# Kernel tuning notes

Hardware: AMD Instinct MI355X
Metric: run time of the kernel (lower is better)

The kernel has to match this reference:

```python
import jax, jax.numpy as jnp
import numpy as np

B, D, H, W = 16, 256, 32, 32
M = 2048


def setup_inputs() -> dict:
    key = jax.random.key(0)
    kz, ke = jax.random.split(key)
    z = jax.random.normal(kz, (B, D, H, W), dtype=jnp.float32)
    e = jax.random.normal(ke, (M, D), dtype=jnp.float32)
    return {"z": z, "e": e}


def reference(z, e):
    # flatten (B, D, H, W) -> (N, D), matching permute(0,2,3,1).reshape(-1, D)
    zf = jnp.transpose(z, (0, 2, 3, 1)).reshape(-1, z.shape[1])  # (N, D)
    # squared L2 distance via GEMM expansion: ||z||^2 + ||e||^2 - 2 z.e^T
    z_sq = jnp.sum(zf * zf, axis=1, keepdims=True)        # (N, 1)
    e_sq = jnp.sum(e * e, axis=1)                          # (M,)
    cross = jnp.einsum('nd,md->nm', zf, e)                 # (N, M)
    distance = jnp.maximum(z_sq + e_sq[None, :] - 2.0 * cross, 0.0)  # (N, M)
    # loss: mean over codes of min over flattened z vectors (min along dim 0)
    loss = jnp.mean(jnp.min(distance, axis=0))
    return distance, loss
```

## Files before the change

### kernel.cpp

```cpp
#include <hip/hip_runtime.h>

typedef __attribute__((ext_vector_type(8))) short bf16x8;
typedef __attribute__((ext_vector_type(4))) float f32x4;

#define NTOT 16384
#define MCODES 2048
#define DDIM 256

__device__ __forceinline__ unsigned short f2bf(float f) {
  union { float f; unsigned u; } v; v.f = f;
  unsigned r = v.u + 0x7FFFu + ((v.u >> 16) & 1u);
  return (unsigned short)(r >> 16);
}
__device__ __forceinline__ float bf2f(unsigned short u) {
  union { unsigned u; float f; } v; v.u = ((unsigned)u) << 16;
  return v.f;
}

#define GLOAD16(gptr, lptr) \
  __builtin_amdgcn_global_load_lds((const __attribute__((address_space(1))) void*)(gptr), \
                                   (__attribute__((address_space(3))) void*)(lptr), 16, 0, 0)

__global__ void prep_e_k(const float* __restrict__ e, unsigned short* __restrict__ ebf,
                         float* __restrict__ esq, unsigned* __restrict__ colmin) {
  int row = blockIdx.x * 4 + (threadIdx.x >> 6);
  int lane = threadIdx.x & 63;
  const float4 v = *(const float4*)(e + (size_t)row * DDIM + lane * 4);
  ushort4 o;
  o.x = f2bf(v.x); o.y = f2bf(v.y); o.z = f2bf(v.z); o.w = f2bf(v.w);
  *(ushort4*)(ebf + (size_t)row * DDIM + lane * 4) = o;
  float s = v.x * v.x + v.y * v.y + v.z * v.z + v.w * v.w;
  #pragma unroll
  for (int off = 32; off; off >>= 1) s += __shfl_xor(s, off, 64);
  if (lane == 0) {
    esq[row] = s;
    colmin[row] = 0x7F800000u;
  }
}

__global__ void transpose_z_k(const float* __restrict__ z, unsigned short* __restrict__ zf) {
  __shared__ float t[64][68];
  const int b = blockIdx.z, d0 = blockIdx.x * 64, hw0 = blockIdx.y * 64;
  const int l16 = threadIdx.x & 15, g = threadIdx.x >> 4;
  const float* src = z + (size_t)b * 262144 + (size_t)d0 * 1024 + hw0;
  #pragma unroll
  for (int it = 0; it < 4; ++it) {
    int dl = it * 16 + g;
    float4 v = *(const float4*)(src + (size_t)dl * 1024 + l16 * 4);
    *(float4*)&t[dl][l16 * 4] = v;
  }
  __syncthreads();
  const int dl4 = (threadIdx.x & 15) * 4, hwl = threadIdx.x >> 4;
  unsigned short* dst = zf + ((size_t)b * 1024 + hw0) * DDIM + d0;
  #pragma unroll
  for (int it = 0; it < 4; ++it) {
    int hw = it * 16 + hwl;
    float a0 = t[dl4 + 0][hw], a1 = t[dl4 + 1][hw];
    float a2 = t[dl4 + 2][hw], a3 = t[dl4 + 3][hw];
    uint2 w;
    w.x = (unsigned)f2bf(a0) | ((unsigned)f2bf(a1) << 16);
    w.y = (unsigned)f2bf(a2) | ((unsigned)f2bf(a3) << 16);
    *(uint2*)(dst + (size_t)hw * DDIM + dl4) = w;
  }
}

__global__ void zsq_k(const unsigned short* __restrict__ zf, float* __restrict__ zsq) {
  int row = blockIdx.x * 4 + (threadIdx.x >> 6);
  int lane = threadIdx.x & 63;
  ushort4 v = *(const ushort4*)(zf + (size_t)row * DDIM + lane * 4);
  float a = bf2f(v.x), b = bf2f(v.y), c = bf2f(v.z), d = bf2f(v.w);
  float s = a * a + b * b + c * c + d * d;
  #pragma unroll
  for (int off = 32; off; off >>= 1) s += __shfl_xor(s, off, 64);
  if (lane == 0) zsq[row] = s;
}

__global__ __launch_bounds__(256) void gemm_k(
    const unsigned short* __restrict__ A,
    const unsigned short* __restrict__ B,
    const float* __restrict__ zsq, const float* __restrict__ esq,
    unsigned* __restrict__ colmin, float* __restrict__ out) {
  __shared__ unsigned short As[128 * 32];
  __shared__ unsigned short Bs[128 * 32];
  const int wave = threadIdx.x >> 6, lane = threadIdx.x & 63;
  const int wm = wave >> 1, wn = wave & 1;
  const int row0 = blockIdx.y * 128, col0 = blockIdx.x * 128;

  f32x4 acc[4][4] = {};

  const int sr = wave * 16 + (lane >> 2);
  const int sc = (lane & 3) * 8;
  const size_t aBase = (size_t)(row0 + sr) * DDIM + sc;
  const size_t bBase = (size_t)(col0 + sr) * DDIM + sc;

  for (int k0 = 0; k0 < DDIM; k0 += 32) {
    GLOAD16(A + aBase + k0, As + wave * 512);
    GLOAD16(A + aBase + k0 + (size_t)64 * DDIM, As + wave * 512 + 64 * 32);
    GLOAD16(B + bBase + k0, Bs + wave * 512);
    GLOAD16(B + bBase + k0 + (size_t)64 * DDIM, Bs + wave * 512 + 64 * 32);
    __syncthreads();

    bf16x8 a[4], b[4];
    #pragma unroll
    for (int i = 0; i < 4; ++i)
      a[i] = *(const bf16x8*)(As + (wm * 64 + i * 16 + (lane & 15)) * 32 + (lane >> 4) * 8);
    #pragma unroll
    for (int j = 0; j < 4; ++j)
      b[j] = *(const bf16x8*)(Bs + (wn * 64 + j * 16 + (lane & 15)) * 32 + (lane >> 4) * 8);
    #pragma unroll
    for (int i = 0; i < 4; ++i)
      #pragma unroll
      for (int j = 0; j < 4; ++j)
        acc[i][j] = __builtin_amdgcn_mfma_f32_16x16x32_bf16(a[i], b[j], acc[i][j], 0, 0, 0);
    __syncthreads();
  }

  const int r0 = lane >> 4, c = lane & 15;
  float cmin[4] = {3.4e38f, 3.4e38f, 3.4e38f, 3.4e38f};
  #pragma unroll
  for (int j = 0; j < 4; ++j) {
    const int col = col0 + wn * 64 + j * 16 + c;
    const float es = esq[col];
    #pragma unroll
    for (int i = 0; i < 4; ++i) {
      const int row = row0 + wm * 64 + i * 16 + r0 * 4;
      const float4 zs = *(const float4*)(zsq + row);
      const float d0 = fmaxf(zs.x + es - 2.0f * acc[i][j][0], 0.0f);
      const float d1 = fmaxf(zs.y + es - 2.0f * acc[i][j][1], 0.0f);
      const float d2 = fmaxf(zs.z + es - 2.0f * acc[i][j][2], 0.0f);
      const float d3 = fmaxf(zs.w + es - 2.0f * acc[i][j][3], 0.0f);
      out[(size_t)(row + 0) * MCODES + col] = d0;
      out[(size_t)(row + 1) * MCODES + col] = d1;
      out[(size_t)(row + 2) * MCODES + col] = d2;
      out[(size_t)(row + 3) * MCODES + col] = d3;
      cmin[j] = fminf(cmin[j], fminf(fminf(d0, d1), fminf(d2, d3)));
    }
  }
  #pragma unroll
  for (int j = 0; j < 4; ++j) {
    float m = cmin[j];
    m = fminf(m, __shfl_xor(m, 16, 64));
    m = fminf(m, __shfl_xor(m, 32, 64));
    if (lane < 16) {
      const int col = col0 + wn * 64 + j * 16 + lane;
      atomicMin(colmin + col, __float_as_uint(m));
    }
  }
}

__global__ void loss_k(const unsigned* __restrict__ colmin, float* __restrict__ loss) {
  __shared__ float sdata[4];
  int t = threadIdx.x;
  float s = 0.0f;
  for (int i = t; i < MCODES; i += 256) s += __uint_as_float(colmin[i]);
  #pragma unroll
  for (int off = 32; off; off >>= 1) s += __shfl_down(s, off, 64);
  if ((t & 63) == 0) sdata[t >> 6] = s;
  __syncthreads();
  if (t == 0) loss[0] = (sdata[0] + sdata[1] + sdata[2] + sdata[3]) * (1.0f / (float)MCODES);
}

extern "C" void kernel_launch(void* const* d_in, const int* in_sizes, int n_in,
                              void* d_out, int out_size, void* d_ws, size_t ws_size,
                              hipStream_t stream) {
  const float* z = (const float*)d_in[0];
  const float* e = (const float*)d_in[1];
  float* out = (float*)d_out;

  float* ws = (float*)d_ws;
  float* zsq = ws;
  float* esq = ws + NTOT;
  unsigned* colmin = (unsigned*)(ws + NTOT + MCODES);
  unsigned short* ebf = (unsigned short*)(ws + NTOT + 2 * MCODES);
  unsigned short* zf = ebf + (size_t)MCODES * DDIM;

  prep_e_k<<<MCODES / 4, 256, 0, stream>>>(e, ebf, esq, colmin);
  transpose_z_k<<<dim3(4, 16, 16), 256, 0, stream>>>(z, zf);
  zsq_k<<<NTOT / 4, 256, 0, stream>>>(zf, zsq);
  gemm_k<<<dim3(MCODES / 128, NTOT / 128), 256, 0, stream>>>(zf, ebf, zsq, esq, colmin, out);
  loss_k<<<1, 256, 0, stream>>>(colmin, out + (size_t)NTOT * MCODES);
}
```

Before: 181.7 us.

## Fuse z-norm into transpose, double-buffer GEMM LDS with swizzle, nontemporal stores

Folds the z squared-norm computation into the transpose kernel, which now accumulates per-row sums with atomicAdd into a zsq buffer zeroed in prep_e_k. This removes a separate kernel launch and a re-read of zf. It also changes the squared norm to use the fp32 values instead of the rounded bf16 ones. The GEMM now uses a double-buffered LDS pipeline with a K tile of 64 and an XOR swizzle against bank conflicts, plus launch bounds for two blocks per CU. Output distances are written with nontemporal stores to avoid polluting the cache with the large output.

Result: no change. 184.6 us (+1.6%).

```diff
diff --git a/kernel.cpp b/kernel.cpp
--- a/kernel.cpp
+++ b/kernel.cpp
@@ -12,17 +12,15 @@
   unsigned r = v.u + 0x7FFFu + ((v.u >> 16) & 1u);
   return (unsigned short)(r >> 16);
 }
-__device__ __forceinline__ float bf2f(unsigned short u) {
-  union { unsigned u; float f; } v; v.u = ((unsigned)u) << 16;
-  return v.f;
-}
 
 #define GLOAD16(gptr, lptr) \
   __builtin_amdgcn_global_load_lds((const __attribute__((address_space(1))) void*)(gptr), \
                                    (__attribute__((address_space(3))) void*)(lptr), 16, 0, 0)
 
 __global__ void prep_e_k(const float* __restrict__ e, unsigned short* __restrict__ ebf,
-                         float* __restrict__ esq, unsigned* __restrict__ colmin) {
+                         float* __restrict__ esq, unsigned* __restrict__ colmin,
+                         float* __restrict__ zsq) {
+  if (blockIdx.x < 64) zsq[blockIdx.x * 256 + threadIdx.x] = 0.0f;
   int row = blockIdx.x * 4 + (threadIdx.x >> 6);
   int lane = threadIdx.x & 63;
   const float4 v = *(const float4*)(e + (size_t)row * DDIM + lane * 4);
@@ -38,82 +36,108 @@
   }
 }
 
-__global__ void transpose_z_k(const float* __restrict__ z, unsigned short* __restrict__ zf) {
-  __shared__ float t[64][68];
+__global__ void trans_zsq_k(const float* __restrict__ z, unsigned short* __restrict__ zf,
+                            float* __restrict__ zsq) {
+  __shared__ float t[64][65];
   const int b = blockIdx.z, d0 = blockIdx.x * 64, hw0 = blockIdx.y * 64;
-  const int l16 = threadIdx.x & 15, g = threadIdx.x >> 4;
-  const float* src = z + (size_t)b * 262144 + (size_t)d0 * 1024 + hw0;
-  #pragma unroll
-  for (int it = 0; it < 4; ++it) {
-    int dl = it * 16 + g;
-    float4 v = *(const float4*)(src + (size_t)dl * 1024 + l16 * 4);
-    *(float4*)&t[dl][l16 * 4] = v;
+  const int tid = threadIdx.x;
+  {
+    const int dl = tid >> 4, hwl = (tid & 15) * 4;
+    const float* src = z + (size_t)b * 262144 + (size_t)(d0 + dl) * 1024 + hw0 + hwl;
+    #pragma unroll
+    for (int it = 0; it < 4; ++it) {
+      float4 v = *(const float4*)(src + (size_t)it * 16 * 1024);
+      *(float4*)&t[it * 16 + dl][hwl] = v;
+    }
   }
   __syncthreads();
-  const int dl4 = (threadIdx.x & 15) * 4, hwl = threadIdx.x >> 4;
-  unsigned short* dst = zf + ((size_t)b * 1024 + hw0) * DDIM + d0;
-  #pragma unroll
-  for (int it = 0; it < 4; ++it) {
-    int hw = it * 16 + hwl;
-    float a0 = t[dl4 + 0][hw], a1 = t[dl4 + 1][hw];
-    float a2 = t[dl4 + 2][hw], a3 = t[dl4 + 3][hw];
-    uint2 w;
-    w.x = (unsigned)f2bf(a0) | ((unsigned)f2bf(a1) << 16);
-    w.y = (unsigned)f2bf(a2) | ((unsigned)f2bf(a3) << 16);
-    *(uint2*)(dst + (size_t)hw * DDIM + dl4) = w;
-  }
-}
-
-__global__ void zsq_k(const unsigned short* __restrict__ zf, float* __restrict__ zsq) {
-  int row = blockIdx.x * 4 + (threadIdx.x >> 6);
-  int lane = threadIdx.x & 63;
-  ushort4 v = *(const ushort4*)(zf + (size_t)row * DDIM + lane * 4);
-  float a = bf2f(v.x), b = bf2f(v.y), c = bf2f(v.z), d = bf2f(v.w);
-  float s = a * a + b * b + c * c + d * d;
-  #pragma unroll
-  for (int off = 32; off; off >>= 1) s += __shfl_xor(s, off, 64);
-  if (lane == 0) zsq[row] = s;
-}
-
-__global__ __launch_bounds__(256) void gemm_k(
+  const int hwl = tid >> 3;
+  const int dl = (tid & 7) * 8;
+  #pragma unroll
+  for (int p = 0; p < 2; ++p) {
+    const int hw = p * 32 + hwl;
+    float vv[8];
+    float s = 0.0f;
+    #pragma unroll
+    for (int u = 0; u < 8; ++u) { vv[u] = t[dl + u][hw]; s += vv[u] * vv[u]; }
+    bf16x8 pk;
+    #pragma unroll
+    for (int u = 0; u < 8; ++u) pk[u] = (short)f2bf(vv[u]);
+    const size_t n = (size_t)b * 1024 + hw0 + hw;
+    *(bf16x8*)(zf + n * DDIM + d0 + dl) = pk;
+    s += __shfl_xor(s, 1, 64);
+    s += __shfl_xor(s, 2, 64);
+    s += __shfl_xor(s, 4, 64);
+    if ((tid & 7) == 0) atomicAdd(zsq + n, s);
+  }
+}
+
+__global__ __launch_bounds__(256, 2) void gemm_k(
     const unsigned short* __restrict__ A,
     const unsigned short* __restrict__ B,
     const float* __restrict__ zsq, const float* __restrict__ esq,
     unsigned* __restrict__ colmin, float* __restrict__ out) {
-  __shared__ unsigned short As[128 * 32];
-  __shared__ unsigned short Bs[128 * 32];
-  const int wave = threadIdx.x >> 6, lane = threadIdx.x & 63;
+  __shared__ unsigned short lds[2][2 * 128 * 64];
+  const int tid = threadIdx.x;
+  const int wave = tid >> 6, lane = tid & 63;
   const int wm = wave >> 1, wn = wave & 1;
   const int row0 = blockIdx.y * 128, col0 = blockIdx.x * 128;
 
+  const int sr = tid >> 3;
+  const int scs = ((tid & 7) * 8) ^ ((sr & 7) * 8);
+  size_t aOff[4], bOff[4];
+  #pragma unroll
+  for (int c = 0; c < 4; ++c) {
+    aOff[c] = (size_t)(row0 + c * 32 + sr) * DDIM + scs;
+    bOff[c] = (size_t)(col0 + c * 32 + sr) * DDIM + scs;
+  }
+
+  const int rA = wm * 64 + (lane & 15);
+  const int rB = wn * 64 + (lane & 15);
+  const int slot = (lane >> 4) * 16;
+  const int swz = (lane & 7) << 4;
+
   f32x4 acc[4][4] = {};
 
-  const int sr = wave * 16 + (lane >> 2);
-  const int sc = (lane & 3) * 8;
-  const size_t aBase = (size_t)(row0 + sr) * DDIM + sc;
-  const size_t bBase = (size_t)(col0 + sr) * DDIM + sc;
-
-  for (int k0 = 0; k0 < DDIM; k0 += 32) {
-    GLOAD16(A + aBase + k0, As + wave * 512);
-    GLOAD16(A + aBase + k0 + (size_t)64 * DDIM, As + wave * 512 + 64 * 32);
-    GLOAD16(B + bBase + k0, Bs + wave * 512);
-    GLOAD16(B + bBase + k0 + (size_t)64 * DDIM, Bs + wave * 512 + 64 * 32);
-    __syncthreads();
-
-    bf16x8 a[4], b[4];
-    #pragma unroll
-    for (int i = 0; i < 4; ++i)
-      a[i] = *(const bf16x8*)(As + (wm * 64 + i * 16 + (lane & 15)) * 32 + (lane >> 4) * 8);
-    #pragma unroll
-    for (int j = 0; j < 4; ++j)
-      b[j] = *(const bf16x8*)(Bs + (wn * 64 + j * 16 + (lane & 15)) * 32 + (lane >> 4) * 8);
-    #pragma unroll
-    for (int i = 0; i < 4; ++i)
+  #define STAGE(buf, k0)                                                    \
+    {                                                                       \
+      unsigned short* la = &lds[buf][0];                                    \
+      unsigned short* lb = &lds[buf][8192];                                 \
+      _Pragma("unroll")                                                     \
+      for (int c = 0; c < 4; ++c) {                                         \
+        GLOAD16(A + aOff[c] + (k0), la + c * 2048 + wave * 512);            \
+        GLOAD16(B + bOff[c] + (k0), lb + c * 2048 + wave * 512);            \
+      }                                                                     \
+    }
+
+  STAGE(0, 0);
+  __syncthreads();
+  #pragma unroll
+  for (int t = 0; t < 4; ++t) {
+    const int cur = t & 1;
+    if (t < 3) STAGE(cur ^ 1, (t + 1) * 64);
+    const char* pA = (const char*)&lds[cur][0];
+    const char* pB = (const char*)&lds[cur][8192];
+    bf16x8 av[2][4], bv[2][4];
+    #pragma unroll
+    for (int kk = 0; kk < 2; ++kk) {
+      #pragma unroll
+      for (int i = 0; i < 4; ++i)
+        av[kk][i] = *(const bf16x8*)(pA + (rA + i * 16) * 128 + ((kk * 64 + slot) ^ swz));
       #pragma unroll
       for (int j = 0; j < 4; ++j)
-        acc[i][j] = __builtin_amdgcn_mfma_f32_16x16x32_bf16(a[i], b[j], acc[i][j], 0, 0, 0);
-    __syncthreads();
-  }
+        bv[kk][j] = *(const bf16x8*)(pB + (rB + j * 16) * 128 + ((kk * 64 + slot) ^ swz));
+    }
+    #pragma unroll
+    for (int kk = 0; kk < 2; ++kk)
+      #pragma unroll
+      for (int i = 0; i < 4; ++i)
+        #pragma unroll
+        for (int j = 0; j < 4; ++j)
+          acc[i][j] = __builtin_amdgcn_mfma_f32_16x16x32_bf16(av[kk][i], bv[kk][j], acc[i][j], 0, 0, 0);
+    if (t < 3) __syncthreads();
+  }
+  #undef STAGE
 
   const int r0 = lane >> 4, c = lane & 15;
   float cmin[4] = {3.4e38f, 3.4e38f, 3.4e38f, 3.4e38f};
@@ -129,10 +153,10 @@
       const float d1 = fmaxf(zs.y + es - 2.0f * acc[i][j][1], 0.0f);
       const float d2 = fmaxf(zs.z + es - 2.0f * acc[i][j][2], 0.0f);
       const float d3 = fmaxf(zs.w + es - 2.0f * acc[i][j][3], 0.0f);
-      out[(size_t)(row + 0) * MCODES + col] = d0;
-      out[(size_t)(row + 1) * MCODES + col] = d1;
-      out[(size_t)(row + 2) * MCODES + col] = d2;
-      out[(size_t)(row + 3) * MCODES + col] = d3;
+      __builtin_nontemporal_store(d0, &out[(size_t)(row + 0) * MCODES + col]);
+      __builtin_nontemporal_store(d1, &out[(size_t)(row + 1) * MCODES + col]);
+      __builtin_nontemporal_store(d2, &out[(size_t)(row + 2) * MCODES + col]);
+      __builtin_nontemporal_store(d3, &out[(size_t)(row + 3) * MCODES + col]);
       cmin[j] = fminf(cmin[j], fminf(fminf(d0, d1), fminf(d2, d3)));
     }
   }
@@ -174,9 +198,8 @@
   unsigned short* ebf = (unsigned short*)(ws + NTOT + 2 * MCODES);
   unsigned short* zf = ebf + (size_t)MCODES * DDIM;
 
-  prep_e_k<<<MCODES / 4, 256, 0, stream>>>(e, ebf, esq, colmin);
-  transpose_z_k<<<dim3(4, 16, 16), 256, 0, stream>>>(z, zf);
-  zsq_k<<<NTOT / 4, 256, 0, stream>>>(zf, zsq);
+  prep_e_k<<<MCODES / 4, 256, 0, stream>>>(e, ebf, esq, colmin, zsq);
+  trans_zsq_k<<<dim3(4, 16, 16), 256, 0, stream>>>(z, zf, zsq);
   gemm_k<<<dim3(MCODES / 128, NTOT / 128), 256, 0, stream>>>(zf, ebf, zsq, esq, colmin, out);
   loss_k<<<1, 256, 0, stream>>>(colmin, out + (size_t)NTOT * MCODES);
 }
```
